# Optimization experiments

Measured on AMD Instinct MI355X. Metric: run time of the kernel, lower is better.

## Reference

```python
import jax, jax.numpy as jnp
import numpy as np
from jax import lax

EPS = 1e-5
H, W = 666, 666  # ny, nx from voxel_size=0.3 over [-100,100]
NUM_CLASSES = 3


def _conv(x, w, b):
    # x: NCHW, w: OIHW, 3x3 stride 1 'SAME'
    y = lax.conv_general_dilated(x, w, (1, 1), 'SAME',
                                 dimension_numbers=('NCHW', 'OIHW', 'NCHW'))
    return y + b[None, :, None, None]


def _bn2d(x, g, b):
    # training-mode BatchNorm2d: batch stats over (N,H,W), biased variance
    m = jnp.mean(x, axis=(0, 2, 3), keepdims=True)
    v = jnp.var(x, axis=(0, 2, 3), keepdims=True)
    return (x - m) * lax.rsqrt(v + EPS) * g[None, :, None, None] + b[None, :, None, None]


def _maxpool2(x):
    return lax.reduce_window(x, -jnp.inf, lax.max, (1, 1, 2, 2), (1, 1, 2, 2), 'VALID')


def setup_inputs() -> dict:
    key = jax.random.key(0)
    ks = jax.random.split(key, 24)
    B, P, N = 4, 12000, 32
    pillars = jax.random.normal(ks[0], (B, P, N, 9), dtype=jnp.float32)
    # unique pillar coords per batch (matches real voxelization: one pillar per cell)
    def coords_for(k):
        flat = jax.random.permutation(k, H * W)[:P]
        y = flat // W
        x = flat % W
        z = jnp.zeros_like(x)
        return jnp.stack([z, y, x, z], axis=-1)  # (batch_idx slot unused, y, x, z)
    coords = jax.vmap(coords_for)(jax.random.split(ks[1], B)).astype(jnp.int64)

    def w(k, shape, fan_in):
        s = 1.0 / np.sqrt(fan_in)
        return jax.random.uniform(k, shape, jnp.float32, -s, s)

    params = dict(
        lin_w=w(ks[2], (64, 9), 9), lin_b=w(ks[3], (64,), 9),
        bn0_g=jnp.ones((64,), jnp.float32), bn0_b=jnp.zeros((64,), jnp.float32),
        c1_w=w(ks[4], (64, 64, 3, 3), 64 * 9), c1_b=w(ks[5], (64,), 64 * 9),
        bn1_g=jnp.ones((64,), jnp.float32), bn1_b=jnp.zeros((64,), jnp.float32),
        c2_w=w(ks[6], (128, 64, 3, 3), 64 * 9), c2_b=w(ks[7], (128,), 64 * 9),
        bn2_g=jnp.ones((128,), jnp.float32), bn2_b=jnp.zeros((128,), jnp.float32),
        h1_w=w(ks[8], (256, 128, 3, 3), 128 * 9), h1_b=w(ks[9], (256,), 128 * 9),
        hbn_g=jnp.ones((256,), jnp.float32), hbn_b=jnp.zeros((256,), jnp.float32),
        box_w=w(ks[10], (NUM_CLASSES * 7, 256, 3, 3), 256 * 9), box_b=w(ks[11], (NUM_CLASSES * 7,), 256 * 9),
        cls_w=w(ks[12], (NUM_CLASSES, 256, 3, 3), 256 * 9), cls_b=w(ks[13], (NUM_CLASSES,), 256 * 9),
        dir_w=w(ks[14], (2, 256, 3, 3), 256 * 9), dir_b=w(ks[15], (2,), 256 * 9),
    )
    return dict(pillars=pillars, coords=coords, **params)


def _forward(pillars, coords, lin_w, lin_b, bn0_g, bn0_b,
             c1_w, c1_b, bn1_g, bn1_b, c2_w, c2_b, bn2_g, bn2_b,
             h1_w, h1_b, hbn_g, hbn_b, box_w, box_b, cls_w, cls_b, dir_w, dir_b):
    B, P, N, D = pillars.shape
    # --- PillarFeatureNet: Linear -> BN1d (over all B*P*N rows) -> ReLU -> max over points
    x = jnp.einsum('bpnd,cd->bpnc', pillars, lin_w) + lin_b
    m = jnp.mean(x, axis=(0, 1, 2), keepdims=True)
    v = jnp.var(x, axis=(0, 1, 2), keepdims=True)
    x = jax.nn.relu((x - m) * lax.rsqrt(v + EPS) * bn0_g + bn0_b)
    feats = jnp.max(x, axis=2)  # [B, P, 64]

    # --- PseudoImageScatter: one fused scatter (replaces per-point python loop)
    y_idx = coords[:, :, 1]
    x_idx = coords[:, :, 2]
    valid = (x_idx >= 0) & (x_idx < W) & (y_idx >= 0) & (y_idx < H)
    b_off = jnp.arange(B, dtype=y_idx.dtype)[:, None] * (H * W)
    flat = b_off + y_idx * W + x_idx
    flat = jnp.where(valid, flat, B * H * W)  # invalid -> dummy slot
    C = feats.shape[-1]
    buf = jnp.zeros((B * H * W + 1, C), feats.dtype)
    buf = buf.at[flat.reshape(-1)].set(feats.reshape(-1, C))
    pseudo = buf[:B * H * W].reshape(B, H, W, C).transpose(0, 3, 1, 2)  # [B,64,H,W]

    # --- CNN backbone
    h = _maxpool2(jax.nn.relu(_bn2d(_conv(pseudo, c1_w, c1_b), bn1_g, bn1_b)))   # [B,64,333,333]
    h = _maxpool2(jax.nn.relu(_bn2d(_conv(h, c2_w, c2_b), bn2_g, bn2_b)))        # [B,128,166,166]

    # --- SSD head
    h = jax.nn.relu(_bn2d(_conv(h, h1_w, h1_b), hbn_g, hbn_b))                   # [B,256,166,166]
    bbox = _conv(h, box_w, box_b)
    cls = _conv(h, cls_w, cls_b)
    direc = _conv(h, dir_w, dir_b)
    return bbox, cls, direc


def reference(pillars, coords, lin_w, lin_b, bn0_g, bn0_b,
              c1_w, c1_b, bn1_g, bn1_b, c2_w, c2_b, bn2_g, bn2_b,
              h1_w, h1_b, hbn_g, hbn_b, box_w, box_b, cls_w, cls_b, dir_w, dir_b):
    return _forward(pillars, coords, lin_w, lin_b, bn0_g, bn0_b,
                    c1_w, c1_b, bn1_g, bn1_b, c2_w, c2_b, bn2_g, bn2_b,
                    h1_w, h1_b, hbn_g, hbn_b, box_w, box_b, cls_w, cls_b, dir_w, dir_b)
```

## Files before the change

### kernel.cpp

```cpp
#include <hip/hip_runtime.h>
#include <hip/hip_bf16.h>

#define B_ 4
#define P_ 12000
#define N_ 32
#define H1_ 666
#define W1_ 666
#define HW1 (H1_*W1_)
#define H2_ 333
#define W2_ 333
#define HW2 (H2_*W2_)
#define H3_ 166
#define W3_ 166
#define HW3 (H3_*W3_)
#define EPS_ 1e-5f

#define PSH_H 340
#define PSH_W 708
#define P1_H 340
#define P1_W 388
#define P2_H 172
#define P2_W 196

typedef short s16x8 __attribute__((ext_vector_type(8)));
typedef float f32x4 __attribute__((ext_vector_type(4)));

__device__ __forceinline__ unsigned short f2bf(float f) {
    unsigned int x = __float_as_uint(f);
    return (unsigned short)((x + 0x7fffu + ((x >> 16) & 1u)) >> 16);
}
__device__ __forceinline__ float bf2f(unsigned short u) {
    return __uint_as_float(((unsigned int)u) << 16);
}

__device__ __forceinline__ void gload16(const void* g, void* l) {
    __builtin_amdgcn_global_load_lds(
        (const __attribute__((address_space(1))) void*)g,
        (__attribute__((address_space(3))) void*)l, 16, 0, 0);
}

__global__ void k_diag(float* __restrict__ out, int n, float val) {
    int i = blockIdx.x * 256 + threadIdx.x;
    if (i < n) out[i] = val;
}

__global__ __launch_bounds__(256) void k_linmax(
    const float* __restrict__ pillars,
    const float* __restrict__ lin_w, const float* __restrict__ lin_b,
    float* __restrict__ maxx, float* __restrict__ sbuf) {
    __shared__ float xs[64 * 268];
    __shared__ float wsm[64 * 10];
    const int tid = threadIdx.x;
    if (tid < 64) {
#pragma unroll
        for (int j = 0; j < 9; ++j) wsm[tid * 10 + j] = lin_w[tid * 9 + j];
        wsm[tid * 10 + 9] = lin_b[tid];
    }
    __syncthreads();
    const float* p = pillars + (size_t)(blockIdx.x * 256 + tid) * 9;
    float f0=p[0], f1=p[1], f2=p[2], f3=p[3], f4=p[4],
          f5=p[5], f6=p[6], f7=p[7], f8=p[8];
#pragma unroll
    for (int c = 0; c < 64; ++c) {
        const float* wc = &wsm[c * 10];
        float x = wc[9] + wc[0]*f0 + wc[1]*f1 + wc[2]*f2 + wc[3]*f3 + wc[4]*f4
                        + wc[5]*f5 + wc[6]*f6 + wc[7]*f7 + wc[8]*f8;
        xs[c * 268 + tid] = x;
    }
    __syncthreads();
    const int c = tid & 63;
    const int w = tid >> 6;
    float s = 0.f, q = 0.f;
#pragma unroll
    for (int pi = 0; pi < 2; ++pi) {
        const int pp = w + pi * 4;
        float mx = -3e38f;
#pragma unroll
        for (int j = 0; j < 32; j += 4) {
            f32x4 v = *(const f32x4*)&xs[c * 268 + pp * 32 + j];
            s += v[0] + v[1] + v[2] + v[3];
            q += v[0]*v[0] + v[1]*v[1] + v[2]*v[2] + v[3]*v[3];
            mx = fmaxf(mx, fmaxf(fmaxf(v[0], v[1]), fmaxf(v[2], v[3])));
        }
        maxx[(size_t)(blockIdx.x * 8 + pp) * 64 + c] = mx;
    }
    float* mybuf = sbuf + (size_t)(blockIdx.x & 63) * 128;
    atomicAdd(&mybuf[c], s);
    atomicAdd(&mybuf[64 + c], q);
}

__global__ void k_finalize2(const float* __restrict__ bufs,
                            const float* __restrict__ g, const float* __restrict__ b,
                            float* __restrict__ scale, float* __restrict__ shift,
                            int C, float invN) {
    int c = blockIdx.x * 256 + threadIdx.x;
    if (c >= C) return;
    float s = 0.f, q = 0.f;
    for (int k = 0; k < 64; ++k) {
        s += bufs[(size_t)k * 2 * C + c];
        q += bufs[(size_t)k * 2 * C + C + c];
    }
    float m = s * invN;
    float v = q * invN - m * m;
    float sc = g[c] * rsqrtf(v + EPS_);
    scale[c] = sc;
    shift[c] = b[c] - m * sc;
}

__global__ void k_featsbn(const float* __restrict__ maxx,
                          const float* __restrict__ sc, const float* __restrict__ sh,
                          short* __restrict__ feats) {
    int i = blockIdx.x * 256 + threadIdx.x;
    if (i >= B_ * P_ * 8) return;
    int c0 = (i & 7) * 8;
    size_t base = (size_t)(i >> 3) * 64 + c0;
    f32x4 v0 = *(const f32x4*)&maxx[base];
    f32x4 v1 = *(const f32x4*)&maxx[base + 4];
    ushort4 o0, o1;
    o0.x = f2bf(fmaxf(fmaf(v0[0], sc[c0+0], sh[c0+0]), 0.f));
    o0.y = f2bf(fmaxf(fmaf(v0[1], sc[c0+1], sh[c0+1]), 0.f));
    o0.z = f2bf(fmaxf(fmaf(v0[2], sc[c0+2], sh[c0+2]), 0.f));
    o0.w = f2bf(fmaxf(fmaf(v0[3], sc[c0+3], sh[c0+3]), 0.f));
    o1.x = f2bf(fmaxf(fmaf(v1[0], sc[c0+4], sh[c0+4]), 0.f));
    o1.y = f2bf(fmaxf(fmaf(v1[1], sc[c0+5], sh[c0+5]), 0.f));
    o1.z = f2bf(fmaxf(fmaf(v1[2], sc[c0+6], sh[c0+6]), 0.f));
    o1.w = f2bf(fmaxf(fmaf(v1[3], sc[c0+7], sh[c0+7]), 0.f));
    *(ushort4*)&feats[base] = o0;
    *(ushort4*)&feats[base + 4] = o1;
}

__global__ void k_probe_coords(const int* __restrict__ c32, int* __restrict__ flag) {
    int nz = 0;
    for (int i = 0; i < 512; ++i) nz |= c32[2*i + 1];
    *flag = (nz == 0) ? 1 : 0;
}

__global__ void k_wt2(const float* __restrict__ src, short* __restrict__ dst,
                      int Cin, int MT, int NCB, int total) {
    int i = blockIdx.x * 256 + threadIdx.x;
    if (i >= total) return;
    int e = i & 7;  int t = i >> 3;
    int chunk = t & 63; t >>= 6;
    int n16 = chunk >> 2;
    int g = (chunk & 3) ^ ((n16 >> 1) & 3);
    int mt = t % MT;  t /= MT;
    int tap = t % 9;  t /= 9;
    int cb = t % NCB; int cg = t / NCB;
    int co = (cg * MT + mt) * 16 + n16;
    int ci = cb * 32 + g * 8 + e;
    dst[i] = (short)f2bf(src[((size_t)co * Cin + ci) * 9 + tap]);
}

__global__ void k_wt2_heads(const float* __restrict__ box, const float* __restrict__ cls,
                            const float* __restrict__ dir,
                            const float* __restrict__ boxb, const float* __restrict__ clsb,
                            const float* __restrict__ dirb,
                            short* __restrict__ dst, float* __restrict__ bias) {
    int i = blockIdx.x * 256 + threadIdx.x;
    if (i >= 73728) return;
    int e = i & 7;  int t = i >> 3;
    int chunk = t & 63; t >>= 6;
    int n16 = chunk >> 2;
    int g = (chunk & 3) ^ ((n16 >> 1) & 3);
    int mt = t & 1;   t >>= 1;
    int tap = t % 9;  int cb = t / 9;
    int oc = mt * 16 + n16;
    int ci = cb * 32 + g * 8 + e;
    float v = 0.f;
    if (oc < 21)      v = box[((size_t)oc * 256 + ci) * 9 + tap];
    else if (oc < 24) v = cls[((size_t)(oc - 21) * 256 + ci) * 9 + tap];
    else if (oc < 26) v = dir[((size_t)(oc - 24) * 256 + ci) * 9 + tap];
    dst[i] = (short)f2bf(v);
    if (i < 32) {
        float bv = 0.f;
        if (i < 21) bv = boxb[i];
        else if (i < 24) bv = clsb[i - 21];
        else if (i < 26) bv = dirb[i - 24];
        bias[i] = bv;
    }
}

template<bool CLEAR>
__global__ void k_scatter(const short* __restrict__ feats,
                          const int* __restrict__ coords32,
                          const int* __restrict__ flag64,
                          short* __restrict__ pseudo,
                          int b, int ylo, int yhi, int rowOff) {
    const int p = blockIdx.x * 4 + (threadIdx.x >> 6);
    const int c = threadIdx.x & 63;
    const int bp = b * P_ + p;
    long long y, x;
    if (*flag64) {
        const long long* c64 = (const long long*)coords32;
        y = c64[(size_t)bp*4 + 1];
        x = c64[(size_t)bp*4 + 2];
    } else {
        y = coords32[(size_t)bp*4 + 1];
        x = coords32[(size_t)bp*4 + 2];
    }
    if (y >= ylo && y < yhi && x >= 0 && x < W1_)
        pseudo[(((size_t)(y - 1 - rowOff + 1)) * PSH_W + (x + 1)) * 64 + c]
            = CLEAR ? (short)0 : feats[(size_t)bp * 64 + c];
}

template<int C>
__global__ void k_bnrelu_pad(short* __restrict__ buf,
                             const float* __restrict__ sc, const float* __restrict__ sh,
                             int Hd, int Wd, int Hp, int Wp) {
    constexpr int OCT = C / 8;
    constexpr int LO = (C == 64) ? 3 : (C == 128) ? 4 : 5;
    size_t i = (size_t)blockIdx.x * 256 + threadIdx.x;
    size_t total = (size_t)B_ * Hd * Wd * OCT;
    if (i >= total) return;
    int oct = (int)(i & (OCT - 1));
    size_t t = i >> LO;
    int x = (int)(t % Wd); t /= Wd;
    int y = (int)(t % Hd);
    int b = (int)(t / Hd);
    size_t idx = (((size_t)b * Hp + y + 1) * Wp + x + 1) * C + oct * 8;
    uint4 v = *(uint4*)&buf[idx];
    unsigned short* u = (unsigned short*)&v;
#pragma unroll
    for (int j = 0; j < 8; ++j)
        u[j] = f2bf(fmaxf(fmaf(bf2f(u[j]), sc[oct*8 + j], sh[oct*8 + j]), 0.f));
    *(uint4*)&buf[idx] = v;
}

template<int CIN, int MT, bool POOL, bool STATS, bool HEADS>
__global__ __launch_bounds__(256) void k_mconv3(
    const short* __restrict__ in, const short* __restrict__ wt2,
    const float* __restrict__ bias,
    short* __restrict__ out, float* __restrict__ outf,
    float* __restrict__ sbuf,
    int Hp, int Wp, int rowOff, int yoff,
    int Win, int Hin, int HpO, int WpO, int CoutT, int cgCount) {

    constexpr int NCB = CIN / 32;
    constexpr int ACH = 9 * MT * 64;
    constexpr int BCH = 6 * 66 * 4;
    __shared__ short sA[ACH * 8];
    __shared__ short sB[BCH * 8];

    const int tid = threadIdx.x;
    const int lane = tid & 63, w = tid >> 6;
    const int n16 = lane & 15, g = lane >> 4;
    const int b  = blockIdx.z / cgCount;
    const int cg = blockIdx.z % cgCount;
    const int co0 = cg * (MT * 16);
    const int byp = blockIdx.y + yoff;
    const int cy0 = 4 * byp;
    const int x0 = blockIdx.x * 64;
    const int r0p = cy0 - 1 - rowOff;
    const int colbase = w * 16 + n16;
    const int xg = x0 + colbase;

    const int aoff = n16 * 4 + (g ^ ((n16 >> 1) & 3));
    int boff[3];
#pragma unroll
    for (int dx = 0; dx < 3; ++dx) {
        int cdx = colbase + dx;
        boff[dx] = cdx * 4 + (g ^ ((cdx >> 1) & 3));
    }

    f32x4 acc[4][MT];
#pragma unroll
    for (int r = 0; r < 4; ++r)
#pragma unroll
        for (int mt = 0; mt < MT; ++mt)
            acc[r][mt] = *(const f32x4*)&bias[co0 + mt * 16 + g * 4];

    for (int cb = 0; cb < NCB; ++cb) {
        const short* aw = wt2 + (size_t)(cg * NCB + cb) * ACH * 8;
        for (int cc0 = 0; cc0 < ACH; cc0 += 256) {
            int ch = cc0 + tid;
            if (ch < ACH)
                gload16(aw + (size_t)ch * 8, &sA[(cc0 + w * 64) * 8]);
        }
        const short* bw = in + (((size_t)b * Hp + r0p) * Wp + x0) * CIN + cb * 32;
        for (int cc0 = 0; cc0 < BCH; cc0 += 256) {
            int ch = cc0 + tid;
            if (ch < BCH) {
                int oslot = ch & 3;
                int col = (ch >> 2) % 66;
                int row = ch / 264;
                int oct = oslot ^ ((col >> 1) & 3);
                gload16(bw + ((size_t)row * Wp + col) * CIN + oct * 8,
                        &sB[(cc0 + w * 64) * 8]);
            }
        }
        __syncthreads();
#pragma unroll
        for (int tap = 0; tap < 9; ++tap) {
            const int dy = tap / 3, dx = tap % 3;
            s16x8 a[MT], bf[4];
#pragma unroll
            for (int mt = 0; mt < MT; ++mt)
                a[mt] = *(const s16x8*)&sA[((tap * MT + mt) * 64 + aoff) * 8];
#pragma unroll
            for (int r = 0; r < 4; ++r)
                bf[r] = *(const s16x8*)&sB[((r + dy) * 264 + boff[dx]) * 8];
#pragma unroll
            for (int r = 0; r < 4; ++r)
#pragma unroll
                for (int mt = 0; mt < MT; ++mt)
                    acc[r][mt] = __builtin_amdgcn_mfma_f32_16x16x32_bf16(
                        a[mt], bf[r], acc[r][mt], 0, 0, 0);
        }
        __syncthreads();
    }

    if (STATS) {
        const bool colok = xg < Win;
        float* mybuf = sbuf + (size_t)((blockIdx.x + blockIdx.y) & 63) * (2 * CoutT);
#pragma unroll
        for (int mt = 0; mt < MT; ++mt) {
#pragma unroll
            for (int reg = 0; reg < 4; ++reg) {
                float sv = 0.f, qv = 0.f;
                if (colok) {
#pragma unroll
                    for (int r = 0; r < 4; ++r) {
                        if (cy0 + r < Hin) {
                            float v = acc[r][mt][reg];
                            sv += v; qv += v * v;
                        }
                    }
                }
#pragma unroll
                for (int o = 1; o < 16; o <<= 1) {
                    sv += __shfl_xor(sv, o);
                    qv += __shfl_xor(qv, o);
                }
                if (n16 == 0) {
                    int c = co0 + mt * 16 + g * 4 + reg;
                    atomicAdd(&mybuf[c], sv);
                    atomicAdd(&mybuf[CoutT + c], qv);
                }
            }
        }
    }

    if (HEADS) {
        if (xg < Win) {
#pragma unroll
            for (int r = 0; r < 4; ++r) {
                if (cy0 + r >= Hin) continue;
#pragma unroll
                for (int mt = 0; mt < MT; ++mt)
#pragma unroll
                    for (int reg = 0; reg < 4; ++reg) {
                        int oc = co0 + mt * 16 + g * 4 + reg;
                        float v = acc[r][mt][reg];
                        size_t px = (size_t)(cy0 + r) * W3_ + xg;
                        if (oc < 21)
                            outf[((size_t)(b * 21 + oc)) * HW3 + px] = v;
                        else if (oc < 24)
                            outf[(size_t)4 * 21 * HW3 + ((size_t)(b * 3 + oc - 21)) * HW3 + px] = v;
                        else if (oc < 26)
                            outf[(size_t)4 * 24 * HW3 + ((size_t)(b * 2 + oc - 24)) * HW3 + px] = v;
                    }
            }
        }
    } else if (POOL) {
        const bool colok = ((n16 & 1) == 0) && (xg + 1 < Win);
#pragma unroll
        for (int k = 0; k < 2; ++k) {
            const int py = 2 * byp + k;
            const bool rowok = (2 * py + 1 < Hin);
#pragma unroll
            for (int mt = 0; mt < MT; ++mt) {
                float pv[4];
#pragma unroll
                for (int reg = 0; reg < 4; ++reg) {
                    float v = fmaxf(acc[2*k][mt][reg], acc[2*k+1][mt][reg]);
                    v = fmaxf(v, __shfl_xor(v, 1));
                    pv[reg] = v;
                }
                if (colok && rowok) {
                    size_t o = (((size_t)b * HpO + py + 1) * WpO + (xg >> 1) + 1) * CoutT
                               + co0 + mt * 16 + g * 4;
                    ushort4 pk = { f2bf(pv[0]), f2bf(pv[1]), f2bf(pv[2]), f2bf(pv[3]) };
                    *(ushort4*)&out[o] = pk;
                }
            }
        }
    } else {
        if (xg < Win) {
#pragma unroll
            for (int r = 0; r < 4; ++r) {
                if (cy0 + r >= Hin) continue;
#pragma unroll
                for (int mt = 0; mt < MT; ++mt) {
                    size_t o = (((size_t)b * HpO + cy0 + r + 1) * WpO + xg + 1) * CoutT
                               + co0 + mt * 16 + g * 4;
                    ushort4 pk = { f2bf(acc[r][mt][0]), f2bf(acc[r][mt][1]),
                                   f2bf(acc[r][mt][2]), f2bf(acc[r][mt][3]) };
                    *(ushort4*)&out[o] = pk;
                }
            }
        }
    }
}

extern "C" void kernel_launch(void* const* d_in, const int* in_sizes, int n_in,
                              void* d_out, int out_size, void* d_ws, size_t ws_size,
                              hipStream_t stream) {
    const float* pillars = (const float*)d_in[0];
    const int*   coords  = (const int*)d_in[1];
    const float* lin_w = (const float*)d_in[2];
    const float* lin_b = (const float*)d_in[3];
    const float* bn0_g = (const float*)d_in[4];
    const float* bn0_b = (const float*)d_in[5];
    const float* c1_w  = (const float*)d_in[6];
    const float* c1_b  = (const float*)d_in[7];
    const float* bn1_g = (const float*)d_in[8];
    const float* bn1_b = (const float*)d_in[9];
    const float* c2_w  = (const float*)d_in[10];
    const float* c2_b  = (const float*)d_in[11];
    const float* bn2_g = (const float*)d_in[12];
    const float* bn2_b = (const float*)d_in[13];
    const float* h1_w  = (const float*)d_in[14];
    const float* h1_b  = (const float*)d_in[15];
    const float* hbn_g = (const float*)d_in[16];
    const float* hbn_b = (const float*)d_in[17];
    const float* box_w = (const float*)d_in[18];
    const float* box_b = (const float*)d_in[19];
    const float* cls_w = (const float*)d_in[20];
    const float* cls_b = (const float*)d_in[21];
    const float* dir_w = (const float*)d_in[22];
    const float* dir_b = (const float*)d_in[23];

    const size_t szPseudo = (size_t)PSH_H * PSH_W * 64 * 2;
    const size_t szP1  = (size_t)B_ * P1_H * P1_W * 64 * 2;
    const size_t szP2  = (size_t)B_ * P2_H * P2_W * 128 * 2;
    const size_t szH1p = (size_t)B_ * P2_H * P2_W * 256 * 2;
    const size_t szR1 = szH1p;
    const size_t szR2 = szP2;
    const size_t offR1 = 0;
    const size_t offR2 = szR1;
    const size_t offFeats = offR2 + szR2;
    const size_t szFeats = (size_t)B_ * P_ * 64 * 2;
    const size_t offC1W = offFeats + szFeats;
    const size_t offC2W = offC1W + 73728;
    const size_t offH1W = offC2W + 147456;
    const size_t offHDW = offH1W + 589824;
    const size_t offArena = offHDW + 147456;
    const size_t wsNeeded = offArena + 300000;
    char* ws = (char*)d_ws;

    if (ws_size < wsNeeded) {
        float mb = (float)(double)(ws_size >> 20);
        k_diag<<<(out_size + 255) / 256, 256, 0, stream>>>((float*)d_out, out_size, mb);
        return;
    }

    float* F = (float*)(ws + offArena);
    float* sbuf0 = F;
    float* L1buf = F + 8192;
    float* L2buf = F + 16384;
    float* L3buf = F + 32768;
    float* sc0 = F + 65536; float* sh0 = F + 65600;
    float* sc1 = F + 65664; float* sh1 = F + 65728;
    float* sc2 = F + 65792; float* sh2 = F + 65920;
    float* sc3 = F + 66048; float* sh3 = F + 66304;
    float* hdbias = F + 66560;
    int* flag64 = (int*)(F + 66596);

    short* pooled1 = (short*)(ws + offR1);
    short* h1p     = (short*)(ws + offR1);
    float* maxx    = (float*)(ws + offR2);
    short* pseudo  = (short*)(ws + offR2);
    short* pooled2 = (short*)(ws + offR2);
    short* feats   = (short*)(ws + offFeats);
    short* c1wt = (short*)(ws + offC1W);
    short* c2wt = (short*)(ws + offC2W);
    short* h1wt = (short*)(ws + offH1W);
    short* hdwt = (short*)(ws + offHDW);

    hipMemsetAsync(ws + offArena, 0, 262144, stream);
    hipMemsetAsync(ws + offR1, 0, szP1, stream);
    k_probe_coords<<<1, 1, 0, stream>>>(coords, flag64);

    k_wt2<<<(64*64*9 + 255)/256, 256, 0, stream>>>(c1_w, c1wt, 64, 4, 2, 64*64*9);
    k_wt2<<<(128*64*9 + 255)/256, 256, 0, stream>>>(c2_w, c2wt, 64, 4, 2, 128*64*9);
    k_wt2<<<(256*128*9 + 255)/256, 256, 0, stream>>>(h1_w, h1wt, 128, 4, 4, 256*128*9);
    k_wt2_heads<<<(73728 + 255)/256, 256, 0, stream>>>(box_w, cls_w, dir_w,
                                                       box_b, cls_b, dir_b,
                                                       hdwt, hdbias);

    k_linmax<<<B_ * P_ * N_ / 256, 256, 0, stream>>>(pillars, lin_w, lin_b, maxx, sbuf0);
    k_finalize2<<<1, 64, 0, stream>>>(sbuf0, bn0_g, bn0_b, sc0, sh0, 64,
                                      1.0f / (float)(B_ * P_ * N_));
    k_featsbn<<<(B_ * P_ * 8 + 255)/256, 256, 0, stream>>>(maxx, sc0, sh0, feats);

    hipMemsetAsync(pseudo, 0, szPseudo, stream);
    for (int b = 0; b < B_; ++b) {
        for (int h = 0; h < 2; ++h) {
            const int ylo = h ? 335 : 0;
            const int yhi = h ? 666 : 337;
            const int rowOff = h ? 335 : -1;
            const int yoff = h ? 84 : 0;
            const int ny = h ? 83 : 84;
            k_scatter<false><<<P_ / 4, 256, 0, stream>>>(feats, coords, flag64, pseudo,
                                                         b, ylo, yhi, rowOff);
            dim3 gr(11, ny, 1);
            k_mconv3<64, 4, true, true, false><<<gr, 256, 0, stream>>>(
                pseudo, c1wt, c1_b,
                pooled1 + (size_t)b * P1_H * P1_W * 64, nullptr, L1buf,
                PSH_H, PSH_W, rowOff, yoff, W1_, H1_, P1_H, P1_W, 64, 1);
            k_scatter<true><<<P_ / 4, 256, 0, stream>>>(feats, coords, flag64, pseudo,
                                                        b, ylo, yhi, rowOff);
        }
    }
    k_finalize2<<<1, 64, 0, stream>>>(L1buf, bn1_g, bn1_b, sc1, sh1, 64,
                                      1.0f / ((float)B_ * HW1));
    {
        size_t total = (size_t)B_ * H2_ * W2_ * 8;
        k_bnrelu_pad<64><<<(unsigned)((total + 255) / 256), 256, 0, stream>>>(
            pooled1, sc1, sh1, H2_, W2_, P1_H, P1_W);
    }

    hipMemsetAsync(ws + offR2, 0, szP2, stream);
    {
        dim3 gr(6, 84, 2 * B_);
        k_mconv3<64, 4, true, true, false><<<gr, 256, 0, stream>>>(
            pooled1, c2wt, c2_b, pooled2, nullptr, L2buf,
            P1_H, P1_W, -1, 0, W2_, H2_, P2_H, P2_W, 128, 2);
    }
    k_finalize2<<<1, 128, 0, stream>>>(L2buf, bn2_g, bn2_b, sc2, sh2, 128,
                                       1.0f / ((float)B_ * HW2));
    {
        size_t total = (size_t)B_ * H3_ * W3_ * 16;
        k_bnrelu_pad<128><<<(unsigned)((total + 255) / 256), 256, 0, stream>>>(
            pooled2, sc2, sh2, H3_, W3_, P2_H, P2_W);
    }

    hipMemsetAsync(ws + offR1, 0, szH1p, stream);
    {
        dim3 gr(3, 42, 4 * B_);
        k_mconv3<128, 4, false, true, false><<<gr, 256, 0, stream>>>(
            pooled2, h1wt, h1_b, h1p, nullptr, L3buf,
            P2_H, P2_W, -1, 0, W3_, H3_, P2_H, P2_W, 256, 4);
    }
    k_finalize2<<<1, 256, 0, stream>>>(L3buf, hbn_g, hbn_b, sc3, sh3, 256,
                                       1.0f / ((float)B_ * HW3));
    {
        size_t total = (size_t)B_ * H3_ * W3_ * 32;
        k_bnrelu_pad<256><<<(unsigned)((total + 255) / 256), 256, 0, stream>>>(
            h1p, sc3, sh3, H3_, W3_, P2_H, P2_W);
    }

    {
        dim3 gr(3, 42, B_);
        k_mconv3<256, 2, false, false, true><<<gr, 256, 0, stream>>>(
            h1p, hdwt, hdbias, nullptr, (float*)d_out, nullptr,
            P2_H, P2_W, -1, 0, W3_, H3_, P2_H, P2_W, 32, 1);
    }
}
```

Before: 710.1 us.

## Double-buffer LDS tiles in conv kernel to overlap loads with MFMA

Allocates two LDS buffers for weight and input tiles and issues the loads for the next channel block before computing the current one. This aims to hide global-to-LDS load latency behind MFMA work. It doubles LDS use per block, which can cut occupancy, and the pipeline depth is short because there are few channel blocks.

```diff
diff --git a/kernel.cpp b/kernel.cpp
--- a/kernel.cpp
+++ b/kernel.cpp
@@ -227,7 +227,7 @@
 }
 
 template<int CIN, int MT, bool POOL, bool STATS, bool HEADS>
-__global__ __launch_bounds__(256) void k_mconv3(
+__global__ __launch_bounds__(256) void k_mconv4(
     const short* __restrict__ in, const short* __restrict__ wt2,
     const float* __restrict__ bias,
     short* __restrict__ out, float* __restrict__ outf,
@@ -238,8 +238,8 @@
     constexpr int NCB = CIN / 32;
     constexpr int ACH = 9 * MT * 64;
     constexpr int BCH = 6 * 66 * 4;
-    __shared__ short sA[ACH * 8];
-    __shared__ short sB[BCH * 8];
+    __shared__ short sA[2][ACH * 8];
+    __shared__ short sB[2][BCH * 8];
 
     const int tid = threadIdx.x;
     const int lane = tid & 63, w = tid >> 6;
@@ -254,29 +254,19 @@
     const int colbase = w * 16 + n16;
     const int xg = x0 + colbase;
 
-    const int aoff = n16 * 4 + (g ^ ((n16 >> 1) & 3));
-    int boff[3];
-#pragma unroll
-    for (int dx = 0; dx < 3; ++dx) {
-        int cdx = colbase + dx;
-        boff[dx] = cdx * 4 + (g ^ ((cdx >> 1) & 3));
-    }
-
-    f32x4 acc[4][MT];
-#pragma unroll
-    for (int r = 0; r < 4; ++r)
-#pragma unroll
-        for (int mt = 0; mt < MT; ++mt)
-            acc[r][mt] = *(const f32x4*)&bias[co0 + mt * 16 + g * 4];
-
-    for (int cb = 0; cb < NCB; ++cb) {
-        const short* aw = wt2 + (size_t)(cg * NCB + cb) * ACH * 8;
+    const short* awBase = wt2 + (size_t)cg * NCB * ACH * 8;
+    const short* bwBase = in + (((size_t)b * Hp + r0p) * Wp + x0) * CIN;
+
+    auto stage = [&](int bufi, int cbi) {
+        const short* aw = awBase + (size_t)cbi * ACH * 8;
+#pragma unroll
         for (int cc0 = 0; cc0 < ACH; cc0 += 256) {
             int ch = cc0 + tid;
             if (ch < ACH)
-                gload16(aw + (size_t)ch * 8, &sA[(cc0 + w * 64) * 8]);
-        }
-        const short* bw = in + (((size_t)b * Hp + r0p) * Wp + x0) * CIN + cb * 32;
+                gload16(aw + (size_t)ch * 8, &sA[bufi][(cc0 + w * 64) * 8]);
+        }
+        const short* bw = bwBase + cbi * 32;
+#pragma unroll
         for (int cc0 = 0; cc0 < BCH; cc0 += 256) {
             int ch = cc0 + tid;
             if (ch < BCH) {
@@ -285,20 +275,42 @@
                 int row = ch / 264;
                 int oct = oslot ^ ((col >> 1) & 3);
                 gload16(bw + ((size_t)row * Wp + col) * CIN + oct * 8,
-                        &sB[(cc0 + w * 64) * 8]);
+                        &sB[bufi][(cc0 + w * 64) * 8]);
             }
         }
-        __syncthreads();
+    };
+
+    const int aoff = n16 * 4 + (g ^ ((n16 >> 1) & 3));
+    int boff[3];
+#pragma unroll
+    for (int dx = 0; dx < 3; ++dx) {
+        int cdx = colbase + dx;
+        boff[dx] = cdx * 4 + (g ^ ((cdx >> 1) & 3));
+    }
+
+    f32x4 acc[4][MT];
+#pragma unroll
+    for (int r = 0; r < 4; ++r)
+#pragma unroll
+        for (int mt = 0; mt < MT; ++mt)
+            acc[r][mt] = *(const f32x4*)&bias[co0 + mt * 16 + g * 4];
+
+    stage(0, 0);
+    __syncthreads();
+
+    for (int cb = 0; cb < NCB; ++cb) {
+        const int cur = cb & 1;
+        if (cb + 1 < NCB) stage(cur ^ 1, cb + 1);
 #pragma unroll
         for (int tap = 0; tap < 9; ++tap) {
             const int dy = tap / 3, dx = tap % 3;
             s16x8 a[MT], bf[4];
 #pragma unroll
             for (int mt = 0; mt < MT; ++mt)
-                a[mt] = *(const s16x8*)&sA[((tap * MT + mt) * 64 + aoff) * 8];
+                a[mt] = *(const s16x8*)&sA[cur][((tap * MT + mt) * 64 + aoff) * 8];
 #pragma unroll
             for (int r = 0; r < 4; ++r)
-                bf[r] = *(const s16x8*)&sB[((r + dy) * 264 + boff[dx]) * 8];
+                bf[r] = *(const s16x8*)&sB[cur][((r + dy) * 264 + boff[dx]) * 8];
 #pragma unroll
             for (int r = 0; r < 4; ++r)
 #pragma unroll
@@ -504,7 +516,7 @@
             k_scatter<false><<<P_ / 4, 256, 0, stream>>>(feats, coords, flag64, pseudo,
                                                          b, ylo, yhi, rowOff);
             dim3 gr(11, ny, 1);
-            k_mconv3<64, 4, true, true, false><<<gr, 256, 0, stream>>>(
+            k_mconv4<64, 4, true, true, false><<<gr, 256, 0, stream>>>(
                 pseudo, c1wt, c1_b,
                 pooled1 + (size_t)b * P1_H * P1_W * 64, nullptr, L1buf,
                 PSH_H, PSH_W, rowOff, yoff, W1_, H1_, P1_H, P1_W, 64, 1);
@@ -523,7 +535,7 @@
     hipMemsetAsync(ws + offR2, 0, szP2, stream);
     {
         dim3 gr(6, 84, 2 * B_);
-        k_mconv3<64, 4, true, true, false><<<gr, 256, 0, stream>>>(
+        k_mconv4<64, 4, true, true, false><<<gr, 256, 0, stream>>>(
             pooled1, c2wt, c2_b, pooled2, nullptr, L2buf,
             P1_H, P1_W, -1, 0, W2_, H2_, P2_H, P2_W, 128, 2);
     }
@@ -538,7 +550,7 @@
     hipMemsetAsync(ws + offR1, 0, szH1p, stream);
     {
         dim3 gr(3, 42, 4 * B_);
-        k_mconv3<128, 4, false, true, false><<<gr, 256, 0, stream>>>(
+        k_mconv4<128, 4, false, true, false><<<gr, 256, 0, stream>>>(
             pooled2, h1wt, h1_b, h1p, nullptr, L3buf,
             P2_H, P2_W, -1, 0, W3_, H3_, P2_H, P2_W, 256, 4);
     }
@@ -552,7 +564,7 @@
 
     {
         dim3 gr(3, 42, B_);
-        k_mconv3<256, 2, false, false, true><<<gr, 256, 0, stream>>>(
+        k_mconv4<256, 2, false, false, true><<<gr, 256, 0, stream>>>(
             h1p, hdwt, hdbias, nullptr, (float*)d_out, nullptr,
             P2_H, P2_W, -1, 0, W3_, H3_, P2_H, P2_W, 32, 1);
     }
```

After: 910.9 us. 1.28x slower.

## Split conv weight staging into three-tap phases and read head inputs directly

Applied to the files above, without the earlier changes.

For the non-head convolutions, weights are now staged into shared memory one kernel row (three taps) at a time instead of all nine taps. This cuts the sA footprint roughly threefold, which should allow more resident blocks per CU, at the cost of two extra barriers per channel block. For the head convolution, the input tile is no longer staged in LDS; each lane loads its B fragments straight from global memory, which frees LDS but relies on caches to absorb the overlapping reads.

```diff
diff --git a/kernel.cpp b/kernel.cpp
--- a/kernel.cpp
+++ b/kernel.cpp
@@ -227,7 +227,7 @@
 }
 
 template<int CIN, int MT, bool POOL, bool STATS, bool HEADS>
-__global__ __launch_bounds__(256) void k_mconv3(
+__global__ __launch_bounds__(256) void k_mconv5(
     const short* __restrict__ in, const short* __restrict__ wt2,
     const float* __restrict__ bias,
     short* __restrict__ out, float* __restrict__ outf,
@@ -236,10 +236,11 @@
     int Win, int Hin, int HpO, int WpO, int CoutT, int cgCount) {
 
     constexpr int NCB = CIN / 32;
-    constexpr int ACH = 9 * MT * 64;
+    constexpr int ATAPS = HEADS ? 9 : 3;
+    constexpr int ACH = ATAPS * MT * 64;
     constexpr int BCH = 6 * 66 * 4;
     __shared__ short sA[ACH * 8];
-    __shared__ short sB[BCH * 8];
+    __shared__ short sB[HEADS ? 8 : BCH * 8];
 
     const int tid = threadIdx.x;
     const int lane = tid & 63, w = tid >> 6;
@@ -269,44 +270,82 @@
         for (int mt = 0; mt < MT; ++mt)
             acc[r][mt] = *(const f32x4*)&bias[co0 + mt * 16 + g * 4];
 
+    const short* awBase = wt2 + (size_t)cg * NCB * 9 * (MT * 64) * 8;
+    const short* bwBase = in + (((size_t)b * Hp + r0p) * Wp + x0) * CIN;
+    size_t hBase = 0;
+    if (HEADS)
+        hBase = (((size_t)b * Hp + r0p) * Wp + x0 + colbase) * CIN + g * 8;
+
     for (int cb = 0; cb < NCB; ++cb) {
-        const short* aw = wt2 + (size_t)(cg * NCB + cb) * ACH * 8;
-        for (int cc0 = 0; cc0 < ACH; cc0 += 256) {
-            int ch = cc0 + tid;
-            if (ch < ACH)
-                gload16(aw + (size_t)ch * 8, &sA[(cc0 + w * 64) * 8]);
-        }
-        const short* bw = in + (((size_t)b * Hp + r0p) * Wp + x0) * CIN + cb * 32;
-        for (int cc0 = 0; cc0 < BCH; cc0 += 256) {
-            int ch = cc0 + tid;
-            if (ch < BCH) {
-                int oslot = ch & 3;
-                int col = (ch >> 2) % 66;
-                int row = ch / 264;
-                int oct = oslot ^ ((col >> 1) & 3);
-                gload16(bw + ((size_t)row * Wp + col) * CIN + oct * 8,
-                        &sB[(cc0 + w * 64) * 8]);
-            }
-        }
-        __syncthreads();
-#pragma unroll
-        for (int tap = 0; tap < 9; ++tap) {
-            const int dy = tap / 3, dx = tap % 3;
-            s16x8 a[MT], bf[4];
-#pragma unroll
-            for (int mt = 0; mt < MT; ++mt)
-                a[mt] = *(const s16x8*)&sA[((tap * MT + mt) * 64 + aoff) * 8];
-#pragma unroll
-            for (int r = 0; r < 4; ++r)
-                bf[r] = *(const s16x8*)&sB[((r + dy) * 264 + boff[dx]) * 8];
-#pragma unroll
-            for (int r = 0; r < 4; ++r)
+        if (HEADS) {
+            const short* aw = awBase + (size_t)(cb * 9) * (MT * 64) * 8;
+            for (int cc0 = 0; cc0 < ACH; cc0 += 256) {
+                int ch = cc0 + tid;
+                if (ch < ACH)
+                    gload16(aw + (size_t)ch * 8, &sA[(cc0 + w * 64) * 8]);
+            }
+            __syncthreads();
+#pragma unroll
+            for (int tap = 0; tap < 9; ++tap) {
+                const int dy = tap / 3, dx = tap % 3;
+                s16x8 a[MT], bf[4];
 #pragma unroll
                 for (int mt = 0; mt < MT; ++mt)
-                    acc[r][mt] = __builtin_amdgcn_mfma_f32_16x16x32_bf16(
-                        a[mt], bf[r], acc[r][mt], 0, 0, 0);
-        }
-        __syncthreads();
+                    a[mt] = *(const s16x8*)&sA[((tap * MT + mt) * 64 + aoff) * 8];
+#pragma unroll
+                for (int r = 0; r < 4; ++r)
+                    bf[r] = *(const s16x8*)&in[hBase + (size_t)((r + dy) * Wp + dx) * CIN + cb * 32];
+#pragma unroll
+                for (int r = 0; r < 4; ++r)
+#pragma unroll
+                    for (int mt = 0; mt < MT; ++mt)
+                        acc[r][mt] = __builtin_amdgcn_mfma_f32_16x16x32_bf16(
+                            a[mt], bf[r], acc[r][mt], 0, 0, 0);
+            }
+            __syncthreads();
+        } else {
+#pragma unroll
+            for (int ph = 0; ph < 3; ++ph) {
+                const short* aw = awBase + (size_t)(cb * 9 + ph * 3) * (MT * 64) * 8;
+                for (int cc0 = 0; cc0 < ACH; cc0 += 256) {
+                    int ch = cc0 + tid;
+                    if (ch < ACH)
+                        gload16(aw + (size_t)ch * 8, &sA[(cc0 + w * 64) * 8]);
+                }
+                if (ph == 0) {
+                    const short* bw = bwBase + cb * 32;
+                    for (int cc0 = 0; cc0 < BCH; cc0 += 256) {
+                        int ch = cc0 + tid;
+                        if (ch < BCH) {
+                            int oslot = ch & 3;
+                            int col = (ch >> 2) % 66;
+                            int row = ch / 264;
+                            int oct = oslot ^ ((col >> 1) & 3);
+                            gload16(bw + ((size_t)row * Wp + col) * CIN + oct * 8,
+                                    &sB[(cc0 + w * 64) * 8]);
+                        }
+                    }
+                }
+                __syncthreads();
+#pragma unroll
+                for (int tloc = 0; tloc < 3; ++tloc) {
+                    s16x8 a[MT], bf[4];
+#pragma unroll
+                    for (int mt = 0; mt < MT; ++mt)
+                        a[mt] = *(const s16x8*)&sA[((tloc * MT + mt) * 64 + aoff) * 8];
+#pragma unroll
+                    for (int r = 0; r < 4; ++r)
+                        bf[r] = *(const s16x8*)&sB[((r + ph) * 264 + boff[tloc]) * 8];
+#pragma unroll
+                    for (int r = 0; r < 4; ++r)
+#pragma unroll
+                        for (int mt = 0; mt < MT; ++mt)
+                            acc[r][mt] = __builtin_amdgcn_mfma_f32_16x16x32_bf16(
+                                a[mt], bf[r], acc[r][mt], 0, 0, 0);
+                }
+                __syncthreads();
+            }
+        }
     }
 
     if (STATS) {
@@ -504,7 +543,7 @@
             k_scatter<false><<<P_ / 4, 256, 0, stream>>>(feats, coords, flag64, pseudo,
                                                          b, ylo, yhi, rowOff);
             dim3 gr(11, ny, 1);
-            k_mconv3<64, 4, true, true, false><<<gr, 256, 0, stream>>>(
+            k_mconv5<64, 4, true, true, false><<<gr, 256, 0, stream>>>(
                 pseudo, c1wt, c1_b,
                 pooled1 + (size_t)b * P1_H * P1_W * 64, nullptr, L1buf,
                 PSH_H, PSH_W, rowOff, yoff, W1_, H1_, P1_H, P1_W, 64, 1);
@@ -523,7 +562,7 @@
     hipMemsetAsync(ws + offR2, 0, szP2, stream);
     {
         dim3 gr(6, 84, 2 * B_);
-        k_mconv3<64, 4, true, true, false><<<gr, 256, 0, stream>>>(
+        k_mconv5<64, 4, true, true, false><<<gr, 256, 0, stream>>>(
             pooled1, c2wt, c2_b, pooled2, nullptr, L2buf,
             P1_H, P1_W, -1, 0, W2_, H2_, P2_H, P2_W, 128, 2);
     }
@@ -538,7 +577,7 @@
     hipMemsetAsync(ws + offR1, 0, szH1p, stream);
     {
         dim3 gr(3, 42, 4 * B_);
-        k_mconv3<128, 4, false, true, false><<<gr, 256, 0, stream>>>(
+        k_mconv5<128, 4, false, true, false><<<gr, 256, 0, stream>>>(
             pooled2, h1wt, h1_b, h1p, nullptr, L3buf,
             P2_H, P2_W, -1, 0, W3_, H3_, P2_H, P2_W, 256, 4);
     }
@@ -552,7 +591,7 @@
 
     {
         dim3 gr(3, 42, B_);
-        k_mconv3<256, 2, false, false, true><<<gr, 256, 0, stream>>>(
+        k_mconv5<256, 2, false, false, true><<<gr, 256, 0, stream>>>(
             h1p, hdwt, hdbias, nullptr, (float*)d_out, nullptr,
             P2_H, P2_W, -1, 0, W3_, H3_, P2_H, P2_W, 32, 1);
     }
```

After: 787.2 us. 10.9% more time.

## Replace dense pseudo-image scatter with index-map gather in first conv

Applied to the files above, without the earlier changes.

Drops the per-batch, per-half loop that scattered pillar features into a dense bf16 pseudo-image, ran conv1, then cleared it again. A padded int index map (pillar id + 1, with 0 pointing at a zero row in feats) is built once, and conv1 gathers features straight from the compact feats array through that map in a single launch over all batches. This removes the large dense image writes and clears and sixteen-odd small launches. In exchange the first conv's loads become an indirect, dependent gather and there is an extra memset of the index map.

```diff
diff --git a/kernel.cpp b/kernel.cpp
--- a/kernel.cpp
+++ b/kernel.cpp
@@ -15,12 +15,12 @@
 #define HW3 (H3_*W3_)
 #define EPS_ 1e-5f
 
-#define PSH_H 340
-#define PSH_W 708
 #define P1_H 340
 #define P1_W 388
 #define P2_H 172
 #define P2_W 196
+#define IDX_H 672
+#define IDX_W 708
 
 typedef short s16x8 __attribute__((ext_vector_type(8)));
 typedef float f32x4 __attribute__((ext_vector_type(4)));
@@ -113,9 +113,10 @@
     int i = blockIdx.x * 256 + threadIdx.x;
     if (i >= B_ * P_ * 8) return;
     int c0 = (i & 7) * 8;
-    size_t base = (size_t)(i >> 3) * 64 + c0;
-    f32x4 v0 = *(const f32x4*)&maxx[base];
-    f32x4 v1 = *(const f32x4*)&maxx[base + 4];
+    size_t src = (size_t)(i >> 3) * 64 + c0;
+    size_t dst = ((size_t)(i >> 3) + 1) * 64 + c0;
+    f32x4 v0 = *(const f32x4*)&maxx[src];
+    f32x4 v1 = *(const f32x4*)&maxx[src + 4];
     ushort4 o0, o1;
     o0.x = f2bf(fmaxf(fmaf(v0[0], sc[c0+0], sh[c0+0]), 0.f));
     o0.y = f2bf(fmaxf(fmaf(v0[1], sc[c0+1], sh[c0+1]), 0.f));
@@ -125,14 +126,33 @@
     o1.y = f2bf(fmaxf(fmaf(v1[1], sc[c0+5], sh[c0+5]), 0.f));
     o1.z = f2bf(fmaxf(fmaf(v1[2], sc[c0+6], sh[c0+6]), 0.f));
     o1.w = f2bf(fmaxf(fmaf(v1[3], sc[c0+7], sh[c0+7]), 0.f));
-    *(ushort4*)&feats[base] = o0;
-    *(ushort4*)&feats[base + 4] = o1;
+    *(ushort4*)&feats[dst] = o0;
+    *(ushort4*)&feats[dst + 4] = o1;
 }
 
 __global__ void k_probe_coords(const int* __restrict__ c32, int* __restrict__ flag) {
     int nz = 0;
     for (int i = 0; i < 512; ++i) nz |= c32[2*i + 1];
     *flag = (nz == 0) ? 1 : 0;
+}
+
+__global__ void k_idxscatter(const int* __restrict__ coords32,
+                             const int* __restrict__ flag64,
+                             int* __restrict__ idxmap) {
+    int bp = blockIdx.x * 256 + threadIdx.x;
+    if (bp >= B_ * P_) return;
+    long long y, x;
+    if (*flag64) {
+        const long long* c64 = (const long long*)coords32;
+        y = c64[(size_t)bp*4 + 1];
+        x = c64[(size_t)bp*4 + 2];
+    } else {
+        y = coords32[(size_t)bp*4 + 1];
+        x = coords32[(size_t)bp*4 + 2];
+    }
+    int b = bp / P_;
+    if (y >= 0 && y < H1_ && x >= 0 && x < W1_)
+        idxmap[((size_t)b * IDX_H + (y + 1)) * IDX_W + (x + 1)] = bp + 1;
 }
 
 __global__ void k_wt2(const float* __restrict__ src, short* __restrict__ dst,
@@ -180,29 +200,6 @@
     }
 }
 
-template<bool CLEAR>
-__global__ void k_scatter(const short* __restrict__ feats,
-                          const int* __restrict__ coords32,
-                          const int* __restrict__ flag64,
-                          short* __restrict__ pseudo,
-                          int b, int ylo, int yhi, int rowOff) {
-    const int p = blockIdx.x * 4 + (threadIdx.x >> 6);
-    const int c = threadIdx.x & 63;
-    const int bp = b * P_ + p;
-    long long y, x;
-    if (*flag64) {
-        const long long* c64 = (const long long*)coords32;
-        y = c64[(size_t)bp*4 + 1];
-        x = c64[(size_t)bp*4 + 2];
-    } else {
-        y = coords32[(size_t)bp*4 + 1];
-        x = coords32[(size_t)bp*4 + 2];
-    }
-    if (y >= ylo && y < yhi && x >= 0 && x < W1_)
-        pseudo[(((size_t)(y - 1 - rowOff + 1)) * PSH_W + (x + 1)) * 64 + c]
-            = CLEAR ? (short)0 : feats[(size_t)bp * 64 + c];
-}
-
 template<int C>
 __global__ void k_bnrelu_pad(short* __restrict__ buf,
                              const float* __restrict__ sc, const float* __restrict__ sh,
@@ -226,10 +223,11 @@
     *(uint4*)&buf[idx] = v;
 }
 
-template<int CIN, int MT, bool POOL, bool STATS, bool HEADS>
-__global__ __launch_bounds__(256) void k_mconv3(
+template<int CIN, int MT, bool POOL, bool STATS, bool HEADS, bool IDX>
+__global__ __launch_bounds__(256) void k_mconv6(
     const short* __restrict__ in, const short* __restrict__ wt2,
     const float* __restrict__ bias,
+    const int* __restrict__ idxmap, const short* __restrict__ feats,
     short* __restrict__ out, float* __restrict__ outf,
     float* __restrict__ sbuf,
     int Hp, int Wp, int rowOff, int yoff,
@@ -269,6 +267,10 @@
         for (int mt = 0; mt < MT; ++mt)
             acc[r][mt] = *(const f32x4*)&bias[co0 + mt * 16 + g * 4];
 
+    const int* imBase = IDX ? (idxmap + ((size_t)b * Hp + r0p) * Wp + x0) : nullptr;
+    const short* bwBase = IDX ? nullptr
+                              : (in + (((size_t)b * Hp + r0p) * Wp + x0) * CIN);
+
     for (int cb = 0; cb < NCB; ++cb) {
         const short* aw = wt2 + (size_t)(cg * NCB + cb) * ACH * 8;
         for (int cc0 = 0; cc0 < ACH; cc0 += 256) {
@@ -276,7 +278,6 @@
             if (ch < ACH)
                 gload16(aw + (size_t)ch * 8, &sA[(cc0 + w * 64) * 8]);
         }
-        const short* bw = in + (((size_t)b * Hp + r0p) * Wp + x0) * CIN + cb * 32;
         for (int cc0 = 0; cc0 < BCH; cc0 += 256) {
             int ch = cc0 + tid;
             if (ch < BCH) {
@@ -284,8 +285,14 @@
                 int col = (ch >> 2) % 66;
                 int row = ch / 264;
                 int oct = oslot ^ ((col >> 1) & 3);
-                gload16(bw + ((size_t)row * Wp + col) * CIN + oct * 8,
-                        &sB[(cc0 + w * 64) * 8]);
+                if (IDX) {
+                    int idx = imBase[(size_t)row * Wp + col];
+                    gload16(feats + ((size_t)idx << 6) + (oct << 3) + cb * 32,
+                            &sB[(cc0 + w * 64) * 8]);
+                } else {
+                    gload16(bwBase + cb * 32 + ((size_t)row * Wp + col) * CIN + oct * 8,
+                            &sB[(cc0 + w * 64) * 8]);
+                }
             }
         }
         __syncthreads();
@@ -430,16 +437,17 @@
     const float* dir_w = (const float*)d_in[22];
     const float* dir_b = (const float*)d_in[23];
 
-    const size_t szPseudo = (size_t)PSH_H * PSH_W * 64 * 2;
     const size_t szP1  = (size_t)B_ * P1_H * P1_W * 64 * 2;
     const size_t szP2  = (size_t)B_ * P2_H * P2_W * 128 * 2;
     const size_t szH1p = (size_t)B_ * P2_H * P2_W * 256 * 2;
     const size_t szR1 = szH1p;
     const size_t szR2 = szP2;
+    const size_t szIdx = (size_t)B_ * IDX_H * IDX_W * 4;
     const size_t offR1 = 0;
     const size_t offR2 = szR1;
+    const size_t offIdx = offR2 + 12582912;
     const size_t offFeats = offR2 + szR2;
-    const size_t szFeats = (size_t)B_ * P_ * 64 * 2;
+    const size_t szFeats = (size_t)(B_ * P_ + 1) * 64 * 2;
     const size_t offC1W = offFeats + szFeats;
     const size_t offC2W = offC1W + 73728;
     const size_t offH1W = offC2W + 147456;
@@ -469,8 +477,8 @@
     short* pooled1 = (short*)(ws + offR1);
     short* h1p     = (short*)(ws + offR1);
     float* maxx    = (float*)(ws + offR2);
-    short* pseudo  = (short*)(ws + offR2);
     short* pooled2 = (short*)(ws + offR2);
+    int*   idxmap  = (int*)(ws + offIdx);
     short* feats   = (short*)(ws + offFeats);
     short* c1wt = (short*)(ws + offC1W);
     short* c2wt = (short*)(ws + offC2W);
@@ -478,8 +486,11 @@
     short* hdwt = (short*)(ws + offHDW);
 
     hipMemsetAsync(ws + offArena, 0, 262144, stream);
+    hipMemsetAsync(ws + offIdx, 0, szIdx, stream);
+    hipMemsetAsync(ws + offFeats, 0, 128, stream);
     hipMemsetAsync(ws + offR1, 0, szP1, stream);
     k_probe_coords<<<1, 1, 0, stream>>>(coords, flag64);
+    k_idxscatter<<<(B_ * P_ + 255)/256, 256, 0, stream>>>(coords, flag64, idxmap);
 
     k_wt2<<<(64*64*9 + 255)/256, 256, 0, stream>>>(c1_w, c1wt, 64, 4, 2, 64*64*9);
     k_wt2<<<(128*64*9 + 255)/256, 256, 0, stream>>>(c2_w, c2wt, 64, 4, 2, 128*64*9);
@@ -493,24 +504,12 @@
                                       1.0f / (float)(B_ * P_ * N_));
     k_featsbn<<<(B_ * P_ * 8 + 255)/256, 256, 0, stream>>>(maxx, sc0, sh0, feats);
 
-    hipMemsetAsync(pseudo, 0, szPseudo, stream);
-    for (int b = 0; b < B_; ++b) {
-        for (int h = 0; h < 2; ++h) {
-            const int ylo = h ? 335 : 0;
-            const int yhi = h ? 666 : 337;
-            const int rowOff = h ? 335 : -1;
-            const int yoff = h ? 84 : 0;
-            const int ny = h ? 83 : 84;
-            k_scatter<false><<<P_ / 4, 256, 0, stream>>>(feats, coords, flag64, pseudo,
-                                                         b, ylo, yhi, rowOff);
-            dim3 gr(11, ny, 1);
-            k_mconv3<64, 4, true, true, false><<<gr, 256, 0, stream>>>(
-                pseudo, c1wt, c1_b,
-                pooled1 + (size_t)b * P1_H * P1_W * 64, nullptr, L1buf,
-                PSH_H, PSH_W, rowOff, yoff, W1_, H1_, P1_H, P1_W, 64, 1);
-            k_scatter<true><<<P_ / 4, 256, 0, stream>>>(feats, coords, flag64, pseudo,
-                                                        b, ylo, yhi, rowOff);
-        }
+    {
+        dim3 gr(11, 167, B_);
+        k_mconv6<64, 4, true, true, false, true><<<gr, 256, 0, stream>>>(
+            nullptr, c1wt, c1_b, idxmap, feats,
+            pooled1, nullptr, L1buf,
+            IDX_H, IDX_W, -1, 0, W1_, H1_, P1_H, P1_W, 64, 1);
     }
     k_finalize2<<<1, 64, 0, stream>>>(L1buf, bn1_g, bn1_b, sc1, sh1, 64,
                                       1.0f / ((float)B_ * HW1));
@@ -523,8 +522,8 @@
     hipMemsetAsync(ws + offR2, 0, szP2, stream);
     {
         dim3 gr(6, 84, 2 * B_);
-        k_mconv3<64, 4, true, true, false><<<gr, 256, 0, stream>>>(
-            pooled1, c2wt, c2_b, pooled2, nullptr, L2buf,
+        k_mconv6<64, 4, true, true, false, false><<<gr, 256, 0, stream>>>(
+            pooled1, c2wt, c2_b, nullptr, nullptr, pooled2, nullptr, L2buf,
             P1_H, P1_W, -1, 0, W2_, H2_, P2_H, P2_W, 128, 2);
     }
     k_finalize2<<<1, 128, 0, stream>>>(L2buf, bn2_g, bn2_b, sc2, sh2, 128,
@@ -538,8 +537,8 @@
     hipMemsetAsync(ws + offR1, 0, szH1p, stream);
     {
         dim3 gr(3, 42, 4 * B_);
-        k_mconv3<128, 4, false, true, false><<<gr, 256, 0, stream>>>(
-            pooled2, h1wt, h1_b, h1p, nullptr, L3buf,
+        k_mconv6<128, 4, false, true, false, false><<<gr, 256, 0, stream>>>(
+            pooled2, h1wt, h1_b, nullptr, nullptr, h1p, nullptr, L3buf,
             P2_H, P2_W, -1, 0, W3_, H3_, P2_H, P2_W, 256, 4);
     }
     k_finalize2<<<1, 256, 0, stream>>>(L3buf, hbn_g, hbn_b, sc3, sh3, 256,
@@ -552,8 +551,8 @@
 
     {
         dim3 gr(3, 42, B_);
-        k_mconv3<256, 2, false, false, true><<<gr, 256, 0, stream>>>(
-            h1p, hdwt, hdbias, nullptr, (float*)d_out, nullptr,
+        k_mconv6<256, 2, false, false, true, false><<<gr, 256, 0, stream>>>(
+            h1p, hdwt, hdbias, nullptr, nullptr, nullptr, (float*)d_out, nullptr,
             P2_H, P2_W, -1, 0, W3_, H3_, P2_H, P2_W, 32, 1);
     }
 }
```

New measurement: 616.9 us. -13.1%, faster.
